# Performance work log

Hardware: AMD Instinct MI355X
Metric: run time of the kernel (lower is better)

The kernel has to match this reference:

```python
import jax, jax.numpy as jnp
import numpy as np

HEADS = 2
BN_EPS = 1e-5


def _axial_self_attn(x, Wq, Wkv, Wout, bout):
    # x: (b, s, t, c) -- attend along t (the axial sequence dim)
    b, s, t, c = x.shape
    dh = c // HEADS
    q = (x @ Wq).reshape(b, s, t, HEADS, dh)
    k, v = jnp.split(x @ Wkv, 2, axis=-1)  # matches torch .chunk(2, dim=-1)
    k = k.reshape(b, s, t, HEADS, dh)
    v = v.reshape(b, s, t, HEADS, dh)
    dots = jnp.einsum('bsind,bsjnd->bsnij', q, k) * (dh ** -0.5)
    attn = jax.nn.softmax(dots, axis=-1)
    out = jnp.einsum('bsnij,bsjnd->bsind', attn, v).reshape(b, s, t, c)
    return out @ Wout + bout


def setup_inputs() -> dict:
    key = jax.random.key(0)
    ks = jax.random.split(key, 8)
    B, C, H, W = 8, 128, 256, 256
    E = 2 * C
    sd = 0.05
    return {
        'x': jax.random.normal(ks[0], (B, C, H, W), jnp.float32),
        'Wq_h': jax.random.normal(ks[1], (C, C), jnp.float32) * sd,
        'Wkv_h': jax.random.normal(ks[2], (C, 2 * C), jnp.float32) * sd,
        'Wout_h': jax.random.normal(ks[3], (C, C), jnp.float32) * sd,
        'bout_h': jnp.zeros((C,), jnp.float32),
        'Wq_w': jax.random.normal(ks[4], (C, C), jnp.float32) * sd,
        'Wkv_w': jax.random.normal(ks[5], (C, 2 * C), jnp.float32) * sd,
        'Wout_w': jax.random.normal(ks[6], (C, C), jnp.float32) * sd,
        'bout_w': jnp.zeros((C,), jnp.float32),
        'conv_w': jax.random.normal(ks[7], (E, E), jnp.float32) * sd,  # (in, out); torch conv weight[o,i,0,0].T
        'gamma': jnp.ones((E,), jnp.float32),
        'beta': jnp.zeros((E,), jnp.float32),
    }


def reference(x, Wq_h, Wkv_h, Wout_h, bout_h, Wq_w, Wkv_w, Wout_w, bout_w, conv_w, gamma, beta):
    B, C, H, W = x.shape
    # MaxPool2d(2)
    xp = x.reshape(B, C, H // 2, 2, W // 2, 2).max(axis=(3, 5))  # (B,C,H2,W2)
    xc = jnp.transpose(xp, (0, 2, 3, 1))  # (B,H2,W2,C) channels-last
    # AxialAttention, sum_axial_out=True: height-axis attn + width-axis attn
    a_h = _axial_self_attn(jnp.transpose(xc, (0, 2, 1, 3)), Wq_h, Wkv_h, Wout_h, bout_h)
    a_h = jnp.transpose(a_h, (0, 2, 1, 3))
    a_w = _axial_self_attn(xc, Wq_w, Wkv_w, Wout_w, bout_w)
    a = jax.nn.relu(a_h + a_w)
    # cat((x_attn, x), dim=channel) then conv1x1 -> relu -> BatchNorm (batch stats)
    y = jnp.concatenate([a, xc], axis=-1) @ conv_w  # (B,H2,W2,2C)
    y = jax.nn.relu(y)
    mean = y.mean(axis=(0, 1, 2))
    var = y.var(axis=(0, 1, 2))
    y = (y - mean) * jax.lax.rsqrt(var + BN_EPS) * gamma + beta
    return jnp.transpose(y, (0, 3, 1, 2))  # back to NCHW
```

## Files before the change

kernel.cpp:

```cpp
#include <hip/hip_runtime.h>
#include <hip/hip_bf16.h>


typedef short v8s __attribute__((ext_vector_type(8)));
typedef short v4s __attribute__((ext_vector_type(4)));
typedef float v4f __attribute__((ext_vector_type(4)));
typedef float v4flt __attribute__((ext_vector_type(4)));

#define LSA 136
#define LSC 264
#define LSY 72
#define LSQ 66

static __device__ __forceinline__ short f2bf(float f){
  __hip_bfloat16 h = __float2bfloat16(f);
  return __builtin_bit_cast(short, h);
}
static __device__ __forceinline__ float bf2f(short s){
  unsigned u = ((unsigned)(unsigned short)s) << 16;
  return __builtin_bit_cast(float, u);
}

__global__ void prep_kernel(const float* __restrict__ Wq_h, const float* __restrict__ Wkv_h,
                            const float* __restrict__ Wout_h, const float* __restrict__ Wq_w,
                            const float* __restrict__ Wkv_w, const float* __restrict__ Wout_w,
                            const float* __restrict__ conv_w, short* __restrict__ wt,
                            float* __restrict__ stats){
  int idx = blockIdx.x * 256 + threadIdx.x;
  if (idx < 8192) stats[idx] = 0.0f;
  const float* src; int K, O, base;
  if      (idx <  16384){ base = 0;      K=128; O=128; src=Wq_h;  }
  else if (idx <  49152){ base = 16384;  K=128; O=256; src=Wkv_h; }
  else if (idx <  65536){ base = 49152;  K=128; O=128; src=Wout_h;}
  else if (idx <  81920){ base = 65536;  K=128; O=128; src=Wq_w;  }
  else if (idx < 114688){ base = 81920;  K=128; O=256; src=Wkv_w; }
  else if (idx < 131072){ base = 114688; K=128; O=128; src=Wout_w;}
  else                  { base = 131072; K=256; O=256; src=conv_w;}
  int local = idx - base;
  int o = local / K, i = local - o * K;
  wt[idx] = f2bf(src[i * O + o]);
}

__global__ __launch_bounds__(256, 8)
void pool_kernel(const float* __restrict__ x, short* __restrict__ xp){
  __shared__ short t_[128*LSQ];
  int bx = blockIdx.x;
  int chalf = bx & 1;
  int row = bx >> 1;
  int b = row >> 7, i = row & 127;
  int tid = (int)threadIdx.x;
  int j2 = tid & 63;
  int cq = tid >> 6;
  for (int rep = 0; rep < 16; ++rep){
    int cl = cq*16 + rep;
    int c = chalf*64 + cl;
    const float* p0 = x + (((b*128 + c)*256 + 2*i)*256 + 4*j2);
    v4flt a  = *(const v4flt*)p0;
    v4flt bb = *(const v4flt*)(p0 + 256);
    t_[(2*j2)*LSQ + cl]   = f2bf(fmaxf(fmaxf(a[0], a[1]), fmaxf(bb[0], bb[1])));
    t_[(2*j2+1)*LSQ + cl] = f2bf(fmaxf(fmaxf(a[2], a[3]), fmaxf(bb[2], bb[3])));
  }
  __syncthreads();
  int obase = ((b*128 + i)*128)*128 + chalf*64;
  #pragma unroll
  for (int rep = 0; rep < 4; ++rep){
    int idx = rep*256 + tid;
    int r_ = idx >> 3, seg = idx & 7;
    *(v8s*)(xp + obase + r_*128 + seg*8) = *(const v8s*)(&t_[r_*LSQ + seg*8]);
  }
}

__global__ __launch_bounds__(512, 6)
void attn_kernel(const short* __restrict__ xp, const short* __restrict__ wt,
                 const float* __restrict__ bout_h, const float* __restrict__ bout_w,
                 short* __restrict__ ah, short* __restrict__ aw){
  __shared__ short A[128*LSA];
  __shared__ short WB[2][32*LSA];

  const int bx = blockIdx.x;
  const int dir = bx & 1;
  const int sb = bx >> 1;
  const int b = sb >> 7, s = sb & 127;
  const int tid = (int)threadIdx.x;
  const int w = tid >> 6;
  const int lane = tid & 63;
  const int l15 = lane & 15, l4 = lane >> 4;
  const int qrow = tid >> 4;
  const int qseg = tid & 15;

  const short* Wq   = wt + dir*65536;
  const short* Wk   = Wq + 16384;
  const short* Wv   = Wq + 32768;
  const short* Wout = Wq + 49152;
  const float* bsrc = dir ? bout_w : bout_h;
  short*       ao   = dir ? aw : ah;

  const int trow = 16*w + l15;
  const int xbase = dir ? (((b*128 + s)*128 + trow)*128)
                        : (((b*128 + trow)*128 + s)*128);
  v8s av[4];
  #pragma unroll
  for (int kk = 0; kk < 4; ++kk)
    av[kk] = *(const v8s*)(xp + xbase + kk*32 + l4*8);

  v8s rw;
#define LOAD_Q(SRC, QI)  rw = *(const v8s*)((SRC) + (32*(QI) + qrow)*128 + qseg*8);
#define WRITE_Q(SL)      *(v8s*)(&WB[SL][qrow*LSA + qseg*8]) = rw;

#define QK_Q(SL, TB)                                                     \
  { _Pragma("unroll")                                                    \
    for (int tcl = 0; tcl < 2; ++tcl){                                   \
      int tc = (TB) + tcl;                                               \
      v4f d = {0.f,0.f,0.f,0.f};                                         \
      _Pragma("unroll")                                                  \
      for (int kk = 0; kk < 4; ++kk){                                    \
        v8s bf = *(const v8s*)(&WB[SL][(tcl*16 + l15)*LSA + kk*32 + l4*8]); \
        d = __builtin_amdgcn_mfma_f32_16x16x32_bf16(av[kk], bf, d, 0, 0, 0); \
      }                                                                  \
      _Pragma("unroll")                                                  \
      for (int r = 0; r < 4; ++r)                                        \
        A[(16*w + 4*l4 + r)*LSA + 16*tc + l15] = f2bf(d[r]);             \
    } }

#define V_Q(SL, TB)                                                      \
  { _Pragma("unroll")                                                    \
    for (int tcl = 0; tcl < 2; ++tcl){                                   \
      int tc = (TB) + tcl;                                               \
      v4f d = {0.f,0.f,0.f,0.f};                                         \
      _Pragma("unroll")                                                  \
      for (int kk = 0; kk < 4; ++kk){                                    \
        v8s bf = *(const v8s*)(&WB[SL][(tcl*16 + l15)*LSA + kk*32 + l4*8]); \
        d = __builtin_amdgcn_mfma_f32_16x16x32_bf16(av[kk], bf, d, 0, 0, 0); \
      }                                                                  \
      v4s pkv;                                                           \
      _Pragma("unroll")                                                  \
      for (int r = 0; r < 4; ++r) pkv[r] = f2bf(d[r]);                   \
      *(v4s*)(&A[(16*tc + l15)*LSA + 16*w + 4*l4]) = pkv;                \
    } }

#define OP_Q(SL, TB)                                                     \
  { _Pragma("unroll")                                                    \
    for (int tcl = 0; tcl < 2; ++tcl){                                   \
      int tc = (TB) + tcl;                                               \
      v4f d = {0.f,0.f,0.f,0.f};                                         \
      _Pragma("unroll")                                                  \
      for (int kk = 0; kk < 4; ++kk){                                    \
        v8s awf = *(const v8s*)(&WB[SL][(tcl*16 + l15)*LSA + kk*32 + l4*8]); \
        d = __builtin_amdgcn_mfma_f32_16x16x32_bf16(awf, ob[kk], d, 0, 0, 0); \
      }                                                                  \
      v4f bias = *(const v4f*)(bsrc + 16*tc + 4*l4);                     \
      v4s z;                                                             \
      _Pragma("unroll")                                                  \
      for (int r = 0; r < 4; ++r) z[r] = f2bf(d[r] + bias[r]);           \
      *(v4s*)(&A[(16*w + l15)*LSA + 16*tc + 4*l4]) = z;                  \
    } }

  LOAD_Q(Wq,0); WRITE_Q(0);
  LOAD_Q(Wq,1);
  __syncthreads();
  QK_Q(0,0); WRITE_Q(1); LOAD_Q(Wq,2);
  __syncthreads();
  QK_Q(1,2); WRITE_Q(0); LOAD_Q(Wq,3);
  __syncthreads();
  QK_Q(0,4); WRITE_Q(1); LOAD_Q(Wk,0);
  __syncthreads();
  QK_Q(1,6); WRITE_Q(0); LOAD_Q(Wk,1);
  v8s bq[2][2];
  #pragma unroll
  for (int h = 0; h < 2; ++h)
    #pragma unroll
    for (int kk = 0; kk < 2; ++kk)
      bq[h][kk] = *(const v8s*)(&A[(16*w + l15)*LSA + h*64 + kk*32 + l4*8]);
  __syncthreads();

  QK_Q(0,0); WRITE_Q(1); LOAD_Q(Wk,2);
  __syncthreads();
  QK_Q(1,2); WRITE_Q(0); LOAD_Q(Wk,3);
  __syncthreads();
  QK_Q(0,4); WRITE_Q(1); LOAD_Q(Wv,0);
  __syncthreads();
  QK_Q(1,6); WRITE_Q(0); LOAD_Q(Wv,1);
  __syncthreads();

  WRITE_Q(1);
  v4s pk[2][8];
  #pragma unroll
  for (int h = 0; h < 2; ++h){
    v4f st[8];
    #pragma unroll
    for (int jt = 0; jt < 8; ++jt){
      v4f d = {0.f,0.f,0.f,0.f};
      #pragma unroll
      for (int kk = 0; kk < 2; ++kk){
        v8s ak = *(const v8s*)(&A[(16*jt + l15)*LSA + h*64 + kk*32 + l4*8]);
        d = __builtin_amdgcn_mfma_f32_16x16x32_bf16(ak, bq[h][kk], d, 0, 0, 0);
      }
      st[jt] = d;
    }
    float mx = -1e30f;
    #pragma unroll
    for (int jt = 0; jt < 8; ++jt)
      #pragma unroll
      for (int r = 0; r < 4; ++r) mx = fmaxf(mx, st[jt][r]);
    mx = fmaxf(mx, __shfl_xor(mx, 16));
    mx = fmaxf(mx, __shfl_xor(mx, 32));
    float sm = 0.f;
    #pragma unroll
    for (int jt = 0; jt < 8; ++jt)
      #pragma unroll
      for (int r = 0; r < 4; ++r){
        float e = __expf((st[jt][r] - mx) * 0.125f);
        st[jt][r] = e; sm += e;
      }
    sm += __shfl_xor(sm, 16);
    sm += __shfl_xor(sm, 32);
    float inv = 1.0f / sm;
    #pragma unroll
    for (int jt = 0; jt < 8; ++jt)
      #pragma unroll
      for (int r = 0; r < 4; ++r) pk[h][jt][r] = f2bf(st[jt][r] * inv);
  }
  LOAD_Q(Wv,2);
  __syncthreads();

  v8s pa[2][4];
  #pragma unroll
  for (int h = 0; h < 2; ++h){
    #pragma unroll
    for (int jt = 0; jt < 8; ++jt)
      *(v4s*)(&A[(16*w + l15)*LSA + 16*jt + 4*l4]) = pk[h][jt];
    #pragma unroll
    for (int kk = 0; kk < 4; ++kk)
      pa[h][kk] = *(const v8s*)(&A[(16*w + l15)*LSA + kk*32 + l4*8]);
  }
  __syncthreads();

  V_Q(0,0);
  __syncthreads();
  V_Q(1,2); WRITE_Q(0); LOAD_Q(Wv,3);
  __syncthreads();
  V_Q(0,4); WRITE_Q(1);
  __syncthreads();
  V_Q(1,6); LOAD_Q(Wout,0);
  __syncthreads();

  WRITE_Q(0);
  v4f ot[2][4];
  #pragma unroll
  for (int h = 0; h < 2; ++h)
    #pragma unroll
    for (int tc = 0; tc < 4; ++tc){
      v4f d = {0.f,0.f,0.f,0.f};
      #pragma unroll
      for (int kk = 0; kk < 4; ++kk){
        v8s vf = *(const v8s*)(&A[(64*h + 16*tc + l15)*LSA + kk*32 + l4*8]);
        d = __builtin_amdgcn_mfma_f32_16x16x32_bf16(vf, pa[h][kk], d, 0, 0, 0);
      }
      ot[h][tc] = d;
    }
  LOAD_Q(Wout,1);
  __syncthreads();

  #pragma unroll
  for (int h = 0; h < 2; ++h)
    #pragma unroll
    for (int tc = 0; tc < 4; ++tc){
      v4s pko;
      #pragma unroll
      for (int r = 0; r < 4; ++r) pko[r] = f2bf(ot[h][tc][r]);
      *(v4s*)(&A[(16*w + l15)*LSA + 64*h + 16*tc + 4*l4]) = pko;
    }
  v8s ob[4];
  #pragma unroll
  for (int kk = 0; kk < 4; ++kk)
    ob[kk] = *(const v8s*)(&A[(16*w + l15)*LSA + kk*32 + l4*8]);
  OP_Q(0,0); WRITE_Q(1); LOAD_Q(Wout,2);
  __syncthreads();
  OP_Q(1,2); WRITE_Q(0); LOAD_Q(Wout,3);
  __syncthreads();
  OP_Q(0,4); WRITE_Q(1);
  __syncthreads();
  OP_Q(1,6);
  __syncthreads();

  int obase = ((b*128 + s)*128)*128;
  #pragma unroll
  for (int r = 0; r < 4; ++r){
    int idx = (r*512 + tid) * 8;
    int t = idx >> 7, c = idx & 127;
    *(v8s*)(ao + obase + t*128 + c) = *(const v8s*)(&A[t*LSA + c]);
  }
#undef LOAD_Q
#undef WRITE_Q
#undef QK_Q
#undef V_Q
#undef OP_Q
}

__global__ __launch_bounds__(512, 4)
void conv_kernel(const short* __restrict__ ah, const short* __restrict__ aw,
                 const short* __restrict__ xp, const short* __restrict__ wt,
                 short* __restrict__ yb, float* __restrict__ stats){
  __shared__ short cats[256*LSY];
  __shared__ float lsum[256];
  __shared__ float lsq[256];
  const short* convT = wt + 131072;
  int bx = blockIdx.x;
  int half = bx & 1;
  int row = bx >> 1;
  int b = row >> 7, ii = row & 127;
  int tid = (int)threadIdx.x;
  int wv = tid >> 6, lane = tid & 63, l15 = lane & 15, l4 = lane >> 4;
  if (tid < 256){ lsum[tid] = 0.f; lsq[tid] = 0.f; }

  v8s wf[2][8];
  #pragma unroll
  for (int x = 0; x < 2; ++x)
    #pragma unroll
    for (int kk = 0; kk < 8; ++kk)
      wf[x][kk] = *(const v8s*)(convT + (((wv + 8*x)*16 + l15)*256) + kk*32 + l4*8);

  #pragma unroll
  for (int r = 0; r < 2; ++r){
    int idx = (r*512 + tid) * 8;
    int t = idx >> 7, c = idx & 127;
    int tg = 64*half + t;
    v8s hv = *(const v8s*)(ah + ((b*128 + tg)*128 + ii)*128 + c);
    v8s wv_ = *(const v8s*)(aw + ((b*128 + ii)*128 + tg)*128 + c);
    v8s o;
    #pragma unroll
    for (int k = 0; k < 8; ++k)
      o[k] = f2bf(fmaxf(bf2f(hv[k]) + bf2f(wv_[k]), 0.f));
    *(v8s*)(&cats[t*LSC + c]) = o;
    *(v8s*)(&cats[t*LSC + 128 + c]) =
        *(const v8s*)(xp + ((b*128 + ii)*128 + tg)*128 + c);
  }
  __syncthreads();

  v4s ypk[2][4];
  float s1[2] = {0.f,0.f}, s2[2] = {0.f,0.f};
  #pragma unroll
  for (int tt = 0; tt < 4; ++tt){
    v4f d0 = {0.f,0.f,0.f,0.f}, d1 = {0.f,0.f,0.f,0.f};
    #pragma unroll
    for (int kk = 0; kk < 8; ++kk){
      v8s af = *(const v8s*)(&cats[(16*tt + l15)*LSC + kk*32 + l4*8]);
      d0 = __builtin_amdgcn_mfma_f32_16x16x32_bf16(af, wf[0][kk], d0, 0, 0, 0);
      d1 = __builtin_amdgcn_mfma_f32_16x16x32_bf16(af, wf[1][kk], d1, 0, 0, 0);
    }
    #pragma unroll
    for (int r = 0; r < 4; ++r){
      float y0 = fmaxf(d0[r], 0.f), y1 = fmaxf(d1[r], 0.f);
      ypk[0][tt][r] = f2bf(y0); ypk[1][tt][r] = f2bf(y1);
      s1[0] += y0; s2[0] += y0*y0;
      s1[1] += y1; s2[1] += y1*y1;
    }
  }
  #pragma unroll
  for (int x = 0; x < 2; ++x){
    s1[x] += __shfl_xor(s1[x], 16); s1[x] += __shfl_xor(s1[x], 32);
    s2[x] += __shfl_xor(s2[x], 16); s2[x] += __shfl_xor(s2[x], 32);
  }
  if (l4 == 0){
    #pragma unroll
    for (int x = 0; x < 2; ++x){
      int e = (wv + 8*x)*16 + l15;
      atomicAdd(&lsum[e], s1[x]);
      atomicAdd(&lsq[e],  s2[x]);
    }
  }
  __syncthreads();
  #pragma unroll
  for (int x = 0; x < 2; ++x)
    #pragma unroll
    for (int tt = 0; tt < 4; ++tt)
      *(v4s*)(&cats[((wv + 8*x)*16 + l15)*LSY + 16*tt + 4*l4]) = ypk[x][tt];
  __syncthreads();
  #pragma unroll
  for (int r = 0; r < 4; ++r){
    int idxv = r*512 + tid;
    int e = idxv >> 3, jseg = idxv & 7;
    *(v8s*)(yb + ((b*256 + e)*128 + ii)*128 + 64*half + jseg*8) =
        *(const v8s*)(&cats[e*LSY + jseg*8]);
  }
  if (tid < 256){
    int c = bx & 15;
    atomicAdd(&stats[c*512 + tid],       lsum[tid]);
    atomicAdd(&stats[c*512 + 256 + tid], lsq[tid]);
  }
}

__global__ void bn_kernel(const short* __restrict__ yb, float* __restrict__ out,
                          const float* __restrict__ stats,
                          const float* __restrict__ gamma, const float* __restrict__ beta){
  const float invn = 1.0f / 131072.0f;
  int bx = blockIdx.x;
  int e = bx & 255;
  float s1 = 0.f, s2 = 0.f;
  #pragma unroll
  for (int c = 0; c < 16; ++c){
    s1 += stats[c*512 + e];
    s2 += stats[c*512 + 256 + e];
  }
  float m   = s1 * invn;
  float var = s2 * invn - m * m;
  float sc  = gamma[e] * rsqrtf(var + 1e-5f);
  float sh  = beta[e] - m * sc;
  int base = bx * 16384;
  int tid = (int)threadIdx.x;
  for (int rep = 0; rep < 8; ++rep){
    int idx = base + (rep*256 + tid)*8;
    v8s yv = *(const v8s*)(yb + idx);
    v4f o1, o2;
    #pragma unroll
    for (int r = 0; r < 4; ++r){
      o1[r] = bf2f(yv[r])   * sc + sh;
      o2[r] = bf2f(yv[4+r]) * sc + sh;
    }
    *(v4f*)(out + idx)     = o1;
    *(v4f*)(out + idx + 4) = o2;
  }
}

extern "C" void kernel_launch(void* const* d_in, const int* in_sizes, int n_in,
                              void* d_out, int out_size, void* d_ws, size_t ws_size,
                              hipStream_t stream){
  const float* x      = (const float*)d_in[0];
  const float* Wq_h   = (const float*)d_in[1];
  const float* Wkv_h  = (const float*)d_in[2];
  const float* Wout_h = (const float*)d_in[3];
  const float* bout_h = (const float*)d_in[4];
  const float* Wq_w   = (const float*)d_in[5];
  const float* Wkv_w  = (const float*)d_in[6];
  const float* Wout_w = (const float*)d_in[7];
  const float* bout_w = (const float*)d_in[8];
  const float* conv_w = (const float*)d_in[9];
  const float* gamma  = (const float*)d_in[10];
  const float* beta   = (const float*)d_in[11];
  float* out = (float*)d_out;

  char* ws = (char*)d_ws;
  short* xp    = (short*)(ws);
  short* ah    = (short*)(ws +  33554432);
  short* aw    = (short*)(ws +  67108864);
  short* yb    = (short*)(ws + 100663296);
  short* wt    = (short*)(ws + 167772160);
  float* stats = (float*)(ws + 168165376);

  prep_kernel<<<768, 256, 0, stream>>>(Wq_h, Wkv_h, Wout_h, Wq_w, Wkv_w, Wout_w,
                                       conv_w, wt, stats);
  pool_kernel<<<2048, 256, 0, stream>>>(x, xp);
  attn_kernel<<<2048, 512, 0, stream>>>(xp, wt, bout_h, bout_w, ah, aw);
  conv_kernel<<<2048, 512, 0, stream>>>(ah, aw, xp, wt, yb, stats);
  bn_kernel<<<2048, 256, 0, stream>>>(yb, out, stats, gamma, beta);
}
```

Measured before the change: 253.7 us.

## Retile attention projections as 2x1 warp tiles sharing weight fragments

Each warp now computes two 16-row tiles for one 16-column output tile instead of one 16-row tile for two column tiles. Each weight fragment read from LDS feeds two MFMAs, halving those LDS reads. The price is more registers for duplicated x fragments, which are reloaded from global memory before the V projection, plus an extra barrier and reordered weight staging.

```diff
diff --git a/kernel.cpp b/kernel.cpp
--- a/kernel.cpp
+++ b/kernel.cpp
@@ -83,6 +83,8 @@
   const int b = sb >> 7, s = sb & 127;
   const int tid = (int)threadIdx.x;
   const int w = tid >> 6;
+  const int m = w >> 1;
+  const int c = w & 1;
   const int lane = tid & 63;
   const int l15 = lane & 15, l4 = lane >> 4;
   const int qrow = tid >> 4;
@@ -95,91 +97,94 @@
   const float* bsrc = dir ? bout_w : bout_h;
   short*       ao   = dir ? aw : ah;
 
-  const int trow = 16*w + l15;
-  const int xbase = dir ? (((b*128 + s)*128 + trow)*128)
-                        : (((b*128 + trow)*128 + s)*128);
-  v8s av[4];
-  #pragma unroll
-  for (int kk = 0; kk < 4; ++kk)
-    av[kk] = *(const v8s*)(xp + xbase + kk*32 + l4*8);
+  const int xb0 = dir ? (((b*128 + s)*128 + (32*m + l15))*128)
+                      : (((b*128 + (32*m + l15))*128 + s)*128);
+  const int xb1 = dir ? (((b*128 + s)*128 + (32*m + 16 + l15))*128)
+                      : (((b*128 + (32*m + 16 + l15))*128 + s)*128);
+  v8s av0[4], av1[4];
+  #pragma unroll
+  for (int kk = 0; kk < 4; ++kk){
+    av0[kk] = *(const v8s*)(xp + xb0 + kk*32 + l4*8);
+    av1[kk] = *(const v8s*)(xp + xb1 + kk*32 + l4*8);
+  }
 
   v8s rw;
 #define LOAD_Q(SRC, QI)  rw = *(const v8s*)((SRC) + (32*(QI) + qrow)*128 + qseg*8);
 #define WRITE_Q(SL)      *(v8s*)(&WB[SL][qrow*LSA + qseg*8]) = rw;
 
-#define QK_Q(SL, TB)                                                     \
-  { _Pragma("unroll")                                                    \
-    for (int tcl = 0; tcl < 2; ++tcl){                                   \
-      int tc = (TB) + tcl;                                               \
-      v4f d = {0.f,0.f,0.f,0.f};                                         \
-      _Pragma("unroll")                                                  \
-      for (int kk = 0; kk < 4; ++kk){                                    \
-        v8s bf = *(const v8s*)(&WB[SL][(tcl*16 + l15)*LSA + kk*32 + l4*8]); \
-        d = __builtin_amdgcn_mfma_f32_16x16x32_bf16(av[kk], bf, d, 0, 0, 0); \
-      }                                                                  \
-      _Pragma("unroll")                                                  \
-      for (int r = 0; r < 4; ++r)                                        \
-        A[(16*w + 4*l4 + r)*LSA + 16*tc + l15] = f2bf(d[r]);             \
+#define QK2(SL, TB)                                                      \
+  { int tc = (TB) + c;                                                   \
+    v4f d0 = {0.f,0.f,0.f,0.f}, d1 = {0.f,0.f,0.f,0.f};                  \
+    _Pragma("unroll")                                                    \
+    for (int kk = 0; kk < 4; ++kk){                                      \
+      v8s bf = *(const v8s*)(&WB[SL][(c*16 + l15)*LSA + kk*32 + l4*8]);  \
+      d0 = __builtin_amdgcn_mfma_f32_16x16x32_bf16(av0[kk], bf, d0, 0, 0, 0); \
+      d1 = __builtin_amdgcn_mfma_f32_16x16x32_bf16(av1[kk], bf, d1, 0, 0, 0); \
+    }                                                                    \
+    _Pragma("unroll")                                                    \
+    for (int r = 0; r < 4; ++r){                                         \
+      A[(32*m + 4*l4 + r)*LSA + 16*tc + l15]      = f2bf(d0[r]);         \
+      A[(32*m + 16 + 4*l4 + r)*LSA + 16*tc + l15] = f2bf(d1[r]);         \
     } }
 
-#define V_Q(SL, TB)                                                      \
-  { _Pragma("unroll")                                                    \
-    for (int tcl = 0; tcl < 2; ++tcl){                                   \
-      int tc = (TB) + tcl;                                               \
-      v4f d = {0.f,0.f,0.f,0.f};                                         \
-      _Pragma("unroll")                                                  \
-      for (int kk = 0; kk < 4; ++kk){                                    \
-        v8s bf = *(const v8s*)(&WB[SL][(tcl*16 + l15)*LSA + kk*32 + l4*8]); \
-        d = __builtin_amdgcn_mfma_f32_16x16x32_bf16(av[kk], bf, d, 0, 0, 0); \
-      }                                                                  \
-      v4s pkv;                                                           \
-      _Pragma("unroll")                                                  \
-      for (int r = 0; r < 4; ++r) pkv[r] = f2bf(d[r]);                   \
-      *(v4s*)(&A[(16*tc + l15)*LSA + 16*w + 4*l4]) = pkv;                \
-    } }
-
-#define OP_Q(SL, TB)                                                     \
-  { _Pragma("unroll")                                                    \
-    for (int tcl = 0; tcl < 2; ++tcl){                                   \
-      int tc = (TB) + tcl;                                               \
-      v4f d = {0.f,0.f,0.f,0.f};                                         \
-      _Pragma("unroll")                                                  \
-      for (int kk = 0; kk < 4; ++kk){                                    \
-        v8s awf = *(const v8s*)(&WB[SL][(tcl*16 + l15)*LSA + kk*32 + l4*8]); \
-        d = __builtin_amdgcn_mfma_f32_16x16x32_bf16(awf, ob[kk], d, 0, 0, 0); \
-      }                                                                  \
-      v4f bias = *(const v4f*)(bsrc + 16*tc + 4*l4);                     \
-      v4s z;                                                             \
-      _Pragma("unroll")                                                  \
-      for (int r = 0; r < 4; ++r) z[r] = f2bf(d[r] + bias[r]);           \
-      *(v4s*)(&A[(16*w + l15)*LSA + 16*tc + 4*l4]) = z;                  \
-    } }
-
-  LOAD_Q(Wq,0); WRITE_Q(0);
-  LOAD_Q(Wq,1);
-  __syncthreads();
-  QK_Q(0,0); WRITE_Q(1); LOAD_Q(Wq,2);
-  __syncthreads();
-  QK_Q(1,2); WRITE_Q(0); LOAD_Q(Wq,3);
-  __syncthreads();
-  QK_Q(0,4); WRITE_Q(1); LOAD_Q(Wk,0);
-  __syncthreads();
-  QK_Q(1,6); WRITE_Q(0); LOAD_Q(Wk,1);
+#define V2(SL, TB)                                                       \
+  { int tc = (TB) + c;                                                   \
+    v4f d0 = {0.f,0.f,0.f,0.f}, d1 = {0.f,0.f,0.f,0.f};                  \
+    _Pragma("unroll")                                                    \
+    for (int kk = 0; kk < 4; ++kk){                                      \
+      v8s bf = *(const v8s*)(&WB[SL][(c*16 + l15)*LSA + kk*32 + l4*8]);  \
+      d0 = __builtin_amdgcn_mfma_f32_16x16x32_bf16(av0[kk], bf, d0, 0, 0, 0); \
+      d1 = __builtin_amdgcn_mfma_f32_16x16x32_bf16(av1[kk], bf, d1, 0, 0, 0); \
+    }                                                                    \
+    v4s p0, p1;                                                          \
+    _Pragma("unroll")                                                    \
+    for (int r = 0; r < 4; ++r){ p0[r] = f2bf(d0[r]); p1[r] = f2bf(d1[r]); } \
+    *(v4s*)(&A[(16*tc + l15)*LSA + 32*m + 4*l4])      = p0;              \
+    *(v4s*)(&A[(16*tc + l15)*LSA + 32*m + 16 + 4*l4]) = p1; }
+
+#define OP2(SL, TB)                                                      \
+  { int tc = (TB) + c;                                                   \
+    v4f d0 = {0.f,0.f,0.f,0.f}, d1 = {0.f,0.f,0.f,0.f};                  \
+    _Pragma("unroll")                                                    \
+    for (int kk = 0; kk < 4; ++kk){                                      \
+      v8s awf = *(const v8s*)(&WB[SL][(c*16 + l15)*LSA + kk*32 + l4*8]); \
+      d0 = __builtin_amdgcn_mfma_f32_16x16x32_bf16(awf, ob0[kk], d0, 0, 0, 0); \
+      d1 = __builtin_amdgcn_mfma_f32_16x16x32_bf16(awf, ob1[kk], d1, 0, 0, 0); \
+    }                                                                    \
+    v4f bias = *(const v4f*)(bsrc + 16*tc + 4*l4);                       \
+    v4s z0, z1;                                                          \
+    _Pragma("unroll")                                                    \
+    for (int r = 0; r < 4; ++r){                                         \
+      z0[r] = f2bf(d0[r] + bias[r]); z1[r] = f2bf(d1[r] + bias[r]); }    \
+    *(v4s*)(&A[(32*m + l15)*LSA + 16*tc + 4*l4])      = z0;              \
+    *(v4s*)(&A[(32*m + 16 + l15)*LSA + 16*tc + 4*l4]) = z1; }
+
+  LOAD_Q(Wq,0); WRITE_Q(0); LOAD_Q(Wq,1);
+  __syncthreads();
+  QK2(0,0); WRITE_Q(1); LOAD_Q(Wq,2);
+  __syncthreads();
+  QK2(1,2); WRITE_Q(0); LOAD_Q(Wq,3);
+  __syncthreads();
+  QK2(0,4); WRITE_Q(1); LOAD_Q(Wk,0);
+  __syncthreads();
+  QK2(1,6);
+  __syncthreads();
   v8s bq[2][2];
   #pragma unroll
   for (int h = 0; h < 2; ++h)
     #pragma unroll
     for (int kk = 0; kk < 2; ++kk)
       bq[h][kk] = *(const v8s*)(&A[(16*w + l15)*LSA + h*64 + kk*32 + l4*8]);
-  __syncthreads();
-
-  QK_Q(0,0); WRITE_Q(1); LOAD_Q(Wk,2);
-  __syncthreads();
-  QK_Q(1,2); WRITE_Q(0); LOAD_Q(Wk,3);
-  __syncthreads();
-  QK_Q(0,4); WRITE_Q(1); LOAD_Q(Wv,0);
-  __syncthreads();
-  QK_Q(1,6); WRITE_Q(0); LOAD_Q(Wv,1);
+  WRITE_Q(0); LOAD_Q(Wk,1);
+  __syncthreads();
+
+  QK2(0,0); WRITE_Q(1); LOAD_Q(Wk,2);
+  __syncthreads();
+  QK2(1,2); WRITE_Q(0); LOAD_Q(Wk,3);
+  __syncthreads();
+  QK2(0,4); WRITE_Q(1); LOAD_Q(Wv,0);
+  __syncthreads();
+  QK2(1,6); WRITE_Q(0); LOAD_Q(Wv,1);
   __syncthreads();
 
   WRITE_Q(1);
@@ -233,15 +238,20 @@
     for (int kk = 0; kk < 4; ++kk)
       pa[h][kk] = *(const v8s*)(&A[(16*w + l15)*LSA + kk*32 + l4*8]);
   }
-  __syncthreads();
-
-  V_Q(0,0);
-  __syncthreads();
-  V_Q(1,2); WRITE_Q(0); LOAD_Q(Wv,3);
-  __syncthreads();
-  V_Q(0,4); WRITE_Q(1);
-  __syncthreads();
-  V_Q(1,6); LOAD_Q(Wout,0);
+  #pragma unroll
+  for (int kk = 0; kk < 4; ++kk){
+    av0[kk] = *(const v8s*)(xp + xb0 + kk*32 + l4*8);
+    av1[kk] = *(const v8s*)(xp + xb1 + kk*32 + l4*8);
+  }
+  __syncthreads();
+
+  V2(0,0);
+  __syncthreads();
+  V2(1,2); WRITE_Q(0); LOAD_Q(Wv,3);
+  __syncthreads();
+  V2(0,4); WRITE_Q(1);
+  __syncthreads();
+  V2(1,6); LOAD_Q(Wout,0);
   __syncthreads();
 
   WRITE_Q(0);
@@ -270,31 +280,37 @@
       for (int r = 0; r < 4; ++r) pko[r] = f2bf(ot[h][tc][r]);
       *(v4s*)(&A[(16*w + l15)*LSA + 64*h + 16*tc + 4*l4]) = pko;
     }
-  v8s ob[4];
-  #pragma unroll
-  for (int kk = 0; kk < 4; ++kk)
-    ob[kk] = *(const v8s*)(&A[(16*w + l15)*LSA + kk*32 + l4*8]);
-  OP_Q(0,0); WRITE_Q(1); LOAD_Q(Wout,2);
-  __syncthreads();
-  OP_Q(1,2); WRITE_Q(0); LOAD_Q(Wout,3);
-  __syncthreads();
-  OP_Q(0,4); WRITE_Q(1);
-  __syncthreads();
-  OP_Q(1,6);
+  __syncthreads();
+
+  v8s ob0[4], ob1[4];
+  #pragma unroll
+  for (int kk = 0; kk < 4; ++kk){
+    ob0[kk] = *(const v8s*)(&A[(32*m + l15)*LSA + kk*32 + l4*8]);
+    ob1[kk] = *(const v8s*)(&A[(32*m + 16 + l15)*LSA + kk*32 + l4*8]);
+  }
+  WRITE_Q(1); LOAD_Q(Wout,2);
+  __syncthreads();
+  OP2(0,0);
+  __syncthreads();
+  OP2(1,2); WRITE_Q(0); LOAD_Q(Wout,3);
+  __syncthreads();
+  OP2(0,4); WRITE_Q(1);
+  __syncthreads();
+  OP2(1,6);
   __syncthreads();
 
   int obase = ((b*128 + s)*128)*128;
   #pragma unroll
   for (int r = 0; r < 4; ++r){
     int idx = (r*512 + tid) * 8;
-    int t = idx >> 7, c = idx & 127;
-    *(v8s*)(ao + obase + t*128 + c) = *(const v8s*)(&A[t*LSA + c]);
+    int t = idx >> 7, cc = idx & 127;
+    *(v8s*)(ao + obase + t*128 + cc) = *(const v8s*)(&A[t*LSA + cc]);
   }
 #undef LOAD_Q
 #undef WRITE_Q
-#undef QK_Q
-#undef V_Q
-#undef OP_Q
+#undef QK2
+#undef V2
+#undef OP2
 }
 
 __global__ __launch_bounds__(512, 4)
```

Result: slower. 272.2 us (+7.3%).
